# Optimization experiments

Measured on AMD Instinct MI355X. Metric: run time of the kernel, lower is better.

## Reference

```python
import jax, jax.numpy as jnp
import numpy as np

B, N, D = 4, 2048, 512
H, DH = 8, 64
MLP = 2048
EPS = 1e-5


def setup_inputs() -> dict:
    key = jax.random.key(0)
    ks = jax.random.split(key, 8)
    s = lambda fan_in: 1.0 / np.sqrt(fan_in)
    return {
        "x": jax.random.normal(ks[0], (B, N, D), jnp.float32),
        "ln1_g": jnp.ones((D,), jnp.float32),
        "ln1_b": jnp.zeros((D,), jnp.float32),
        "Wqkv": jax.random.normal(ks[1], (D, 3 * H * DH), jnp.float32) * s(D),
        "temperature": jnp.asarray(np.log(DH ** -0.5), jnp.float32),
        "Wo": jax.random.normal(ks[2], (H * DH, D), jnp.float32) * s(H * DH),
        "bo": jnp.zeros((D,), jnp.float32),
        "ln2_g": jnp.ones((D,), jnp.float32),
        "ln2_b": jnp.zeros((D,), jnp.float32),
        "W1": jax.random.normal(ks[3], (D, MLP), jnp.float32) * s(D),
        "b1": jnp.zeros((MLP,), jnp.float32),
        "W2": jax.random.normal(ks[4], (MLP, D), jnp.float32) * s(MLP),
        "b2": jnp.zeros((D,), jnp.float32),
    }


def _layernorm(x, g, b):
    mu = jnp.mean(x, axis=-1, keepdims=True)
    var = jnp.var(x, axis=-1, keepdims=True)
    return (x - mu) * jax.lax.rsqrt(var + EPS) * g + b


def _lsa(x, Wqkv, temperature, Wo, bo):
    b, n, _ = x.shape
    qkv = x @ Wqkv  # [b, n, 3*H*DH]
    q, k, v = jnp.split(qkv, 3, axis=-1)
    rs = lambda t: t.reshape(b, n, H, DH).transpose(0, 2, 1, 3)  # b h n d
    q, k, v = rs(q), rs(k), rs(v)
    dots = jnp.einsum("bhnd,bhmd->bhnm", q, k) * jnp.exp(temperature)
    mask_value = -jnp.finfo(dots.dtype).max
    eye = jnp.eye(n, dtype=bool)
    dots = jnp.where(eye, mask_value, dots)  # mask diagonal (LSA)
    attn = jax.nn.softmax(dots, axis=-1)
    out = jnp.einsum("bhnm,bhmd->bhnd", attn, v)
    out = out.transpose(0, 2, 1, 3).reshape(b, n, H * DH)
    return out @ Wo + bo


def _ffn(x, W1, b1, W2, b2):
    h = jax.nn.gelu(x @ W1 + b1, approximate=False)
    return h @ W2 + b2


def reference(x, ln1_g, ln1_b, Wqkv, temperature, Wo, bo,
              ln2_g, ln2_b, W1, b1, W2, b2):
    y = _lsa(_layernorm(x, ln1_g, ln1_b), Wqkv, temperature, Wo, bo) + x
    z = _ffn(_layernorm(y, ln2_g, ln2_b), W1, b1, W2, b2) + y
    return (z, x)
```

## Files before the change

### kernel.cpp

```cpp
#include <hip/hip_runtime.h>
#include <math.h>

typedef __attribute__((ext_vector_type(4))) float f32x4;
typedef __attribute__((ext_vector_type(8))) short short8;

#define DEV __device__ __forceinline__

DEV short f2bf(float f){
  union { float f; unsigned u; } v; v.f = f;
  unsigned r = v.u + 0x7fffu + ((v.u >> 16) & 1u);
  return (short)(r >> 16);
}
DEV float bf2f(short s){
  union { unsigned u; float f; } v; v.u = ((unsigned)(unsigned short)s) << 16; return v.f;
}
DEV float exp2_hw(float x){ float r; asm("v_exp_f32 %0, %1" : "=v"(r) : "v"(x)); return r; }
DEV float rcp_hw(float x){ float r; asm("v_rcp_f32 %0, %1" : "=v"(r) : "v"(x)); return r; }
DEV unsigned cvtpk(float a, float b){
  unsigned r; asm("v_cvt_pk_bf16_f32 %0, %1, %2" : "=v"(r) : "v"(a), "v"(b)); return r;
}
DEV void gload_lds16(const short* src, short* lds){
  __builtin_amdgcn_global_load_lds(
      (const __attribute__((address_space(1))) void*)src,
      (__attribute__((address_space(3))) void*)lds, 16, 0, 0);
}
DEV float gelu_fast(float v){
  float u = v * (0.79788456f + 0.03567741f * v * v);
  float e = exp2_hw(u * 2.88539008f);
  float th = 1.0f - 2.0f * rcp_hw(e + 1.0f);
  return 0.5f * v * (1.0f + th);
}

__global__ __launch_bounds__(256) void transpose_bf16_kernel(
    const float* __restrict__ W, short* __restrict__ Wt, int K, int N)
{
  __shared__ float tile[32][33];
  int nb = blockIdx.x * 32, kb = blockIdx.y * 32;
  int tx = threadIdx.x & 31, ty = threadIdx.x >> 5;
  #pragma unroll
  for (int i = ty; i < 32; i += 8)
    tile[i][tx] = W[(size_t)(kb + i) * N + nb + tx];
  __syncthreads();
  #pragma unroll
  for (int i = ty; i < 32; i += 8)
    Wt[(size_t)(nb + i) * K + kb + tx] = f2bf(tile[tx][i]);
}

template<int COPYX>
__global__ __launch_bounds__(256) void ln_kernel(
    const float* __restrict__ x, const float* __restrict__ g,
    const float* __restrict__ b, short* __restrict__ out,
    float* __restrict__ xcopy)
{
  int row  = blockIdx.x * 4 + (threadIdx.x >> 6);
  int lane = threadIdx.x & 63;
  const float* xr = x + (size_t)row * 512 + lane * 8;
  f32x4 v0 = *(const f32x4*)(xr);
  f32x4 v1 = *(const f32x4*)(xr + 4);
  float s  = (v0[0]+v0[1]+v0[2]+v0[3]) + (v1[0]+v1[1]+v1[2]+v1[3]);
  float sq = (v0[0]*v0[0]+v0[1]*v0[1]+v0[2]*v0[2]+v0[3]*v0[3])
           + (v1[0]*v1[0]+v1[1]*v1[1]+v1[2]*v1[2]+v1[3]*v1[3]);
  #pragma unroll
  for (int off = 1; off < 64; off <<= 1) {
    s  += __shfl_xor(s, off);
    sq += __shfl_xor(sq, off);
  }
  float mu  = s * (1.0f / 512.0f);
  float var = sq * (1.0f / 512.0f) - mu * mu;
  float rstd = rsqrtf(var + 1e-5f);
  f32x4 g0 = *(const f32x4*)(g + lane * 8);
  f32x4 g1 = *(const f32x4*)(g + lane * 8 + 4);
  f32x4 b0 = *(const f32x4*)(b + lane * 8);
  f32x4 b1 = *(const f32x4*)(b + lane * 8 + 4);
  float o[8];
  #pragma unroll
  for (int j = 0; j < 4; ++j) o[j]     = (v0[j] - mu) * rstd * g0[j] + b0[j];
  #pragma unroll
  for (int j = 0; j < 4; ++j) o[4 + j] = (v1[j] - mu) * rstd * g1[j] + b1[j];
  uint4 pk;
  pk.x = cvtpk(o[0], o[1]); pk.y = cvtpk(o[2], o[3]);
  pk.z = cvtpk(o[4], o[5]); pk.w = cvtpk(o[6], o[7]);
  *(uint4*)(out + (size_t)row * 512 + lane * 8) = pk;
  if (COPYX) {
    float* xc = xcopy + (size_t)row * 512 + lane * 8;
    *(f32x4*)(xc)     = v0;
    *(f32x4*)(xc + 4) = v1;
  }
}

__global__ __launch_bounds__(256) void ln_bf_kernel(
    const short* __restrict__ x, const float* __restrict__ g,
    const float* __restrict__ b, short* __restrict__ out)
{
  int row  = blockIdx.x * 4 + (threadIdx.x >> 6);
  int lane = threadIdx.x & 63;
  short8 raw = *(const short8*)(x + (size_t)row * 512 + lane * 8);
  float v[8];
  #pragma unroll
  for (int j = 0; j < 8; ++j) v[j] = bf2f(raw[j]);
  float s = 0.f, sq = 0.f;
  #pragma unroll
  for (int j = 0; j < 8; ++j) { s += v[j]; sq += v[j] * v[j]; }
  #pragma unroll
  for (int off = 1; off < 64; off <<= 1) {
    s  += __shfl_xor(s, off);
    sq += __shfl_xor(sq, off);
  }
  float mu  = s * (1.0f / 512.0f);
  float var = sq * (1.0f / 512.0f) - mu * mu;
  float rstd = rsqrtf(var + 1e-5f);
  f32x4 g0 = *(const f32x4*)(g + lane * 8);
  f32x4 g1 = *(const f32x4*)(g + lane * 8 + 4);
  f32x4 b0 = *(const f32x4*)(b + lane * 8);
  f32x4 b1 = *(const f32x4*)(b + lane * 8 + 4);
  float o[8];
  #pragma unroll
  for (int j = 0; j < 4; ++j) o[j]     = (v[j] - mu) * rstd * g0[j] + b0[j];
  #pragma unroll
  for (int j = 0; j < 4; ++j) o[4 + j] = (v[4+j] - mu) * rstd * g1[j] + b1[j];
  uint4 pk;
  pk.x = cvtpk(o[0], o[1]); pk.y = cvtpk(o[2], o[3]);
  pk.z = cvtpk(o[4], o[5]); pk.w = cvtpk(o[6], o[7]);
  *(uint4*)(out + (size_t)row * 512 + lane * 8) = pk;
}

template<int EPI, int BM, typename OutT>
__global__ __launch_bounds__(256) void gemm_bt_kernel(
    const short* __restrict__ A, const short* __restrict__ Bt,
    OutT* __restrict__ C, const float* __restrict__ bias,
    const float* __restrict__ resid, const short* __restrict__ residb,
    short* __restrict__ vt, int M, int N, int K)
{
  constexpr int MFR = BM / 32;
  constexpr int NFR = 4;
  constexpr int AI  = BM / 64;
  constexpr int BUF = BM * 32 + 128 * 32;
  __shared__ __align__(16) short smem[3 * BUF];

  int tid = threadIdx.x;
  int lane = tid & 63, wid = tid >> 6;
  int l16 = lane & 15, lq = lane >> 4;

  int gx = gridDim.x;
  int nwg = gx * gridDim.y;
  int orig = blockIdx.y * gx + blockIdx.x;
  int swz = (orig & 7) * (nwg >> 3) + (orig >> 3);
  int bn = swz % gx, bm = swz / gx;

  int wm = wid >> 1, wn = wid & 1;

  const short* gaP[AI];
  const short* gbP[2];
  #pragma unroll
  for (int i = 0; i < AI; ++i) {
    int gg = i * 4 + wid;
    gaP[i] = A + (size_t)(bm * BM + gg * 16 + l16) * K + lq * 8;
  }
  #pragma unroll
  for (int i = 0; i < 2; ++i) {
    int gg = i * 4 + wid;
    gbP[i] = Bt + (size_t)(bn * 128 + gg * 16 + l16) * K + lq * 8;
  }

  auto STAGE = [&](int bufi, int k0) {
    short* base = smem + bufi * BUF;
    #pragma unroll
    for (int i = 0; i < AI; ++i)
      gload_lds16(gaP[i] + k0, base + (i * 4 + wid) * 512);
    #pragma unroll
    for (int i = 0; i < 2; ++i)
      gload_lds16(gbP[i] + k0, base + BM * 32 + (i * 4 + wid) * 512);
  };

  f32x4 acc[MFR][NFR] = {};

  STAGE(0, 0);
  STAGE(1, 32);

  int nt = K >> 5;
  for (int t = 0; t < nt; ++t) {
    if (t + 1 < nt) {
      if constexpr (AI == 2) asm volatile("s_waitcnt vmcnt(4)" ::: "memory");
      else                   asm volatile("s_waitcnt vmcnt(3)" ::: "memory");
    } else {
      asm volatile("s_waitcnt vmcnt(0)" ::: "memory");
    }
    __builtin_amdgcn_s_barrier();
    __builtin_amdgcn_sched_barrier(0);
    if (t + 2 < nt) STAGE((t + 2) % 3, (t + 2) << 5);

    const short* base = smem + (t % 3) * BUF;
    short8 af[MFR], bfr[NFR];
    #pragma unroll
    for (int m = 0; m < MFR; ++m)
      af[m] = *(const short8*)(base + (wm * MFR + m) * 512 + lane * 8);
    #pragma unroll
    for (int n = 0; n < NFR; ++n)
      bfr[n] = *(const short8*)(base + BM * 32 + (wn * NFR + n) * 512 + lane * 8);
    __builtin_amdgcn_s_setprio(1);
    #pragma unroll
    for (int m = 0; m < MFR; ++m)
      #pragma unroll
      for (int n = 0; n < NFR; ++n)
        acc[m][n] = __builtin_amdgcn_mfma_f32_16x16x32_bf16(af[m], bfr[n], acc[m][n], 0, 0, 0);
    __builtin_amdgcn_s_setprio(0);
  }

  if (EPI == 3 && bn >= 8) {
    __syncthreads();
    short* T = smem;
    #pragma unroll
    for (int m = 0; m < MFR; ++m)
      #pragma unroll
      for (int n = 0; n < NFR; ++n) {
        int c = wn * 64 + n * 16 + l16;
        #pragma unroll
        for (int r = 0; r < 4; ++r) {
          int rowl = wm * 64 + m * 16 + lq * 4 + r;
          T[c * 128 + (rowl ^ ((c & 7) << 4))] = f2bf(acc[m][n][r]);
        }
      }
    __syncthreads();
    int b2 = bm >> 4;
    int nnb = (bm & 15) * 128;
    int tn = tid & 15;
    #pragma unroll
    for (int c8 = 0; c8 < 8; ++c8) {
      int c = c8 * 16 + (tid >> 4);
      short8 v = *(const short8*)(T + c * 128 + ((tn * 8) ^ ((c & 7) << 4)));
      if (tn & 1) {
        short8 w;
        #pragma unroll
        for (int j = 0; j < 8; ++j) w[j] = v[j ^ 4];
        v = w;
      }
      int c2 = bn * 128 + c - 1024;
      int bh = b2 * 8 + (c2 >> 6);
      int d  = c2 & 63;
      *(short8*)(vt + ((size_t)(bh * 64 + d)) * 2048 + nnb + tn * 8) = v;
    }
    return;
  }

  float bv[NFR];
  #pragma unroll
  for (int n = 0; n < NFR; ++n)
    bv[n] = (EPI == 0 || EPI == 3) ? 0.0f : bias[bn * 128 + (wn * NFR + n) * 16 + l16];

  #pragma unroll
  for (int m = 0; m < MFR; ++m) {
    #pragma unroll
    for (int r = 0; r < 4; ++r) {
      int row = bm * BM + (wm * MFR + m) * 16 + lq * 4 + r;
      #pragma unroll
      for (int n = 0; n < NFR; ++n) {
        int col = bn * 128 + (wn * NFR + n) * 16 + l16;
        float v = acc[m][n][r];
        if (EPI == 2 || EPI == 4 || EPI == 5) v += bv[n];
        if (EPI == 2) v = gelu_fast(v);
        if (EPI == 4) v += resid[(size_t)row * N + col];
        if (EPI == 5) v += bf2f(residb[(size_t)row * N + col]);
        if constexpr (sizeof(OutT) == 2)
          ((short*)C)[(size_t)row * N + col] = f2bf(v);
        else
          ((float*)C)[(size_t)row * N + col] = v;
      }
    }
  }
}

__global__ __launch_bounds__(256, 2) void attn_kernel(
    const short* __restrict__ qkv, const short* __restrict__ vt,
    const float* __restrict__ temp_ptr,
    short* __restrict__ Op0, short* __restrict__ Op1, float* __restrict__ Lbuf)
{
  __shared__ __align__(16) short smem[16384];

  int tid = threadIdx.x;
  int lane = tid & 63, wid = tid >> 6;
  int l16 = lane & 15, lq = lane >> 4;
  int hi = lq >> 1, lq0 = lq & 1;

  int orig = blockIdx.y * 16 + blockIdx.x;
  int swz = (orig & 7) * 128 + (orig >> 3);
  int qb = swz & 15;
  int rr = swz >> 4;
  int bh = rr & 31, slice = rr >> 5;
  int b = bh >> 3, h = bh & 7;

  const short* qbase = qkv + (size_t)b * 2048 * 1536 + h * 64;
  const short* kbase = qbase + 512;
  const short* vbase = vt + (size_t)bh * 64 * 2048;
  int kslice = slice * 1024;

  float scale = __expf(temp_ptr[0]) * 1.44269504f;
  int q0 = qb * 128 + wid * 32;

  short8 qfrag[2][2];
  #pragma unroll
  for (int qf = 0; qf < 2; ++qf) {
    int qrow = q0 + qf * 16 + l16;
    #pragma unroll
    for (int c = 0; c < 2; ++c) {
      short8 raw = *(const short8*)(qbase + (size_t)qrow * 1536 + c * 32 + lq * 8);
      short8 sc;
      #pragma unroll
      for (int j = 0; j < 8; ++j) sc[j] = f2bf(bf2f(raw[j]) * scale);
      qfrag[qf][c] = sc;
    }
  }

  f32x4 accO[2][4] = {};
  float l[2] = {0.f, 0.f};

  auto STAGE = [&](int bufi, int k0) {
    #pragma unroll
    for (int i = 0; i < 2; ++i) {
      int w16 = i * 256 + tid;
      int sub = w16 >> 7;
      int cc  = (w16 >> 6) & 1;
      int lq2 = (w16 >> 4) & 3;
      int l2  = w16 & 15;
      const short* srcK = kbase + (size_t)(k0 + sub * 16 + l2) * 1536 + cc * 32 + lq2 * 8;
      gload_lds16(srcK, smem + bufi * 4096 + (i * 4 + wid) * 512);
      const short* srcV = vbase + (size_t)(sub * 16 + l2) * 2048 + k0 + cc * 32 + lq2 * 8;
      gload_lds16(srcV, smem + 8192 + bufi * 4096 + (i * 4 + wid) * 512);
    }
  };

  STAGE(0, kslice);
  asm volatile("s_waitcnt vmcnt(0)");
  __syncthreads();

  for (int t = 0; t < 16; ++t) {
    int cur = t & 1;
    int k0 = kslice + t * 64;
    if (t + 1 < 16) STAGE(cur ^ 1, k0 + 64);

    const short* kls = smem + cur * 4096;
    const short* vls = smem + 8192 + cur * 4096;

    f32x4 accS[2][4] = {};
    #pragma unroll
    for (int s = 0; s < 4; ++s) {
      short8 kf0 = *(const short8*)(kls + (s * 2 + 0) * 512 + lane * 8);
      short8 kf1 = *(const short8*)(kls + (s * 2 + 1) * 512 + lane * 8);
      #pragma unroll
      for (int qf = 0; qf < 2; ++qf) {
        accS[qf][s] = __builtin_amdgcn_mfma_f32_16x16x32_bf16(kf0, qfrag[qf][0], accS[qf][s], 0, 0, 0);
        accS[qf][s] = __builtin_amdgcn_mfma_f32_16x16x32_bf16(kf1, qfrag[qf][1], accS[qf][s], 0, 0, 0);
      }
    }

    if ((q0 & ~63) == k0) {
      #pragma unroll
      for (int qf = 0; qf < 2; ++qf) {
        int qg = q0 + qf * 16 + l16;
        #pragma unroll
        for (int s = 0; s < 4; ++s)
          #pragma unroll
          for (int r = 0; r < 4; ++r)
            if (k0 + s * 16 + lq * 4 + r == qg) accS[qf][s][r] = -30000.f;
      }
    }

    short8 pa[2][2];
    #pragma unroll
    for (int qf = 0; qf < 2; ++qf) {
      float sum = 0.f;
      unsigned W[4][2];
      #pragma unroll
      for (int s = 0; s < 4; ++s) {
        float p0 = exp2_hw(accS[qf][s][0]);
        float p1 = exp2_hw(accS[qf][s][1]);
        float p2 = exp2_hw(accS[qf][s][2]);
        float p3 = exp2_hw(accS[qf][s][3]);
        sum += (p0 + p1) + (p2 + p3);
        W[s][0] = cvtpk(p0, p1);
        W[s][1] = cvtpk(p2, p3);
      }
      sum += __shfl_xor(sum, 16);
      sum += __shfl_xor(sum, 32);
      l[qf] += sum;

      unsigned K0[2], S0[2], K2[2], S2[2], R0[2], R2[2];
      #pragma unroll
      for (int w = 0; w < 2; ++w) {
        K0[w] = hi ? W[1][w] : W[0][w];
        S0[w] = hi ? W[0][w] : W[1][w];
        K2[w] = hi ? W[3][w] : W[2][w];
        S2[w] = hi ? W[2][w] : W[3][w];
      }
      #pragma unroll
      for (int w = 0; w < 2; ++w) {
        R0[w] = (unsigned)__shfl_xor((int)S0[w], 32);
        R2[w] = (unsigned)__shfl_xor((int)S2[w], 32);
      }
      bool sw = (hi != lq0);
      unsigned FA[2], FB[2], sA[2], sB[2], GA[2], GB[2];
      #pragma unroll
      for (int w = 0; w < 2; ++w) {
        sA[w] = sw ? K0[w] : R0[w];  FA[w] = sw ? R0[w] : K0[w];
        sB[w] = sw ? K2[w] : R2[w];  FB[w] = sw ? R2[w] : K2[w];
      }
      #pragma unroll
      for (int w = 0; w < 2; ++w) {
        GA[w] = (unsigned)__shfl_xor((int)sA[w], 16);
        GB[w] = (unsigned)__shfl_xor((int)sB[w], 16);
      }
      union { unsigned u[4]; short8 s8; } p0u, p1u;
      p0u.u[0] = FA[0]; p0u.u[1] = FA[1]; p0u.u[2] = GA[0]; p0u.u[3] = GA[1];
      p1u.u[0] = FB[0]; p1u.u[1] = FB[1]; p1u.u[2] = GB[0]; p1u.u[3] = GB[1];
      pa[qf][0] = p0u.s8;
      pa[qf][1] = p1u.s8;
    }

    short8 vfr[4][2];
    #pragma unroll
    for (int d = 0; d < 4; ++d) {
      vfr[d][0] = *(const short8*)(vls + (d * 2 + 0) * 512 + lane * 8);
      vfr[d][1] = *(const short8*)(vls + (d * 2 + 1) * 512 + lane * 8);
    }
    #pragma unroll
    for (int qf = 0; qf < 2; ++qf)
      #pragma unroll
      for (int d = 0; d < 4; ++d) {
        accO[qf][d] = __builtin_amdgcn_mfma_f32_16x16x32_bf16(vfr[d][0], pa[qf][0], accO[qf][d], 0, 0, 0);
        accO[qf][d] = __builtin_amdgcn_mfma_f32_16x16x32_bf16(vfr[d][1], pa[qf][1], accO[qf][d], 0, 0, 0);
      }

    __syncthreads();
  }

  short* op = slice ? Op1 : Op0;
  #pragma unroll
  for (int qf = 0; qf < 2; ++qf) {
    int qg = q0 + qf * 16 + l16;
    if (lq == 0) Lbuf[(size_t)(slice * 32 + bh) * 2048 + qg] = l[qf];
    size_t rowoff = (size_t)(b * 2048 + qg) * 512 + h * 64;
    #pragma unroll
    for (int d = 0; d < 4; ++d) {
      unsigned w0 = cvtpk(accO[qf][d][0], accO[qf][d][1]);
      unsigned w1 = cvtpk(accO[qf][d][2], accO[qf][d][3]);
      uint2 pk; pk.x = w0; pk.y = w1;
      *(uint2*)(op + rowoff + d * 16 + lq * 4) = pk;
    }
  }
}

__global__ __launch_bounds__(256) void attn_combine_kernel(
    const short* __restrict__ Op0, const short* __restrict__ Op1,
    const float* __restrict__ Lbuf, short* __restrict__ out)
{
  int idx = blockIdx.x * 256 + threadIdx.x;
  size_t e = (size_t)idx * 8;
  int row = (int)(e >> 9);
  int col = (int)(e & 511);
  int b = row >> 11, q = row & 2047;
  int bh = b * 8 + (col >> 6);
  float l0 = Lbuf[(size_t)bh * 2048 + q];
  float l1 = Lbuf[(size_t)(32 + bh) * 2048 + q];
  float inv = rcp_hw(l0 + l1);
  short8 a = *(const short8*)(Op0 + e);
  short8 c = *(const short8*)(Op1 + e);
  float o[8];
  #pragma unroll
  for (int j = 0; j < 8; ++j) o[j] = (bf2f(a[j]) + bf2f(c[j])) * inv;
  uint4 pk;
  pk.x = cvtpk(o[0], o[1]); pk.y = cvtpk(o[2], o[3]);
  pk.z = cvtpk(o[4], o[5]); pk.w = cvtpk(o[6], o[7]);
  *(uint4*)(out + e) = pk;
}

extern "C" void kernel_launch(void* const* d_in, const int* in_sizes, int n_in,
                              void* d_out, int out_size, void* d_ws, size_t ws_size,
                              hipStream_t stream)
{
  const float* x    = (const float*)d_in[0];
  const float* ln1g = (const float*)d_in[1];
  const float* ln1b = (const float*)d_in[2];
  const float* Wqkv = (const float*)d_in[3];
  const float* temp = (const float*)d_in[4];
  const float* Wo   = (const float*)d_in[5];
  const float* bo   = (const float*)d_in[6];
  const float* ln2g = (const float*)d_in[7];
  const float* ln2b = (const float*)d_in[8];
  const float* W1   = (const float*)d_in[9];
  const float* b1   = (const float*)d_in[10];
  const float* W2   = (const float*)d_in[11];
  const float* b2   = (const float*)d_in[12];
  float* out = (float*)d_out;

  char* ws = (char*)d_ws;
  short* wqkv_t = (short*)(ws);
  float* lpart  = (float*)(ws);
  short* wo_t   = (short*)(ws + 1572864);
  short* w1_t   = (short*)(ws + 2097152);
  short* w2_t   = (short*)(ws + 4194304);
  short* h      = (short*)(ws + 6291456);
  short* qkv    = (short*)(ws + 14680064);
  short* attn   = (short*)(ws + 39845888);
  short* ybf    = (short*)(ws + 48234496);
  short* vt     = (short*)(ws + 48234496);
  short* t      = (short*)(ws + 14680064);

  const int M = 8192;

  transpose_bf16_kernel<<<dim3(1536 / 32, 512 / 32),  256, 0, stream>>>(Wqkv, wqkv_t, 512, 1536);
  transpose_bf16_kernel<<<dim3(512 / 32, 512 / 32),   256, 0, stream>>>(Wo,   wo_t,   512, 512);
  transpose_bf16_kernel<<<dim3(2048 / 32, 512 / 32),  256, 0, stream>>>(W1,   w1_t,   512, 2048);
  transpose_bf16_kernel<<<dim3(512 / 32, 2048 / 32),  256, 0, stream>>>(W2,   w2_t,   2048, 512);

  ln_kernel<1><<<M / 4, 256, 0, stream>>>(x, ln1g, ln1b, h, out + (size_t)M * 512);

  gemm_bt_kernel<3, 128, short><<<dim3(1536 / 128, M / 128), 256, 0, stream>>>(
      h, wqkv_t, qkv, nullptr, nullptr, nullptr, vt, M, 1536, 512);

  attn_kernel<<<dim3(16, 64), 256, 0, stream>>>(qkv, vt, temp, attn, h, lpart);
  attn_combine_kernel<<<M * 512 / 8 / 256, 256, 0, stream>>>(attn, h, lpart, attn);

  gemm_bt_kernel<4, 64, short><<<dim3(512 / 128, M / 64), 256, 0, stream>>>(
      attn, wo_t, ybf, bo, x, nullptr, nullptr, M, 512, 512);

  ln_bf_kernel<<<M / 4, 256, 0, stream>>>(ybf, ln2g, ln2b, h);

  gemm_bt_kernel<2, 128, short><<<dim3(2048 / 128, M / 128), 256, 0, stream>>>(
      h, w1_t, t, b1, nullptr, nullptr, nullptr, M, 2048, 512);

  gemm_bt_kernel<5, 64, float><<<dim3(512 / 128, M / 64), 256, 0, stream>>>(
      t, w2_t, out, b2, nullptr, ybf, nullptr, M, 512, 2048);
}
```

Before: 210.1 us.

## Add 256x128-tile, 512-thread GEMM kernel for QKV and FFN1 projections

Adds a new GEMM kernel with 256x128 output tiles, 8 waves and a K-step of 64 with triple-buffered LDS staging. It is used for the QKV projection (including the V-transpose epilogue) and for the FFN up-projection with GELU. The old kernel keeps only the bias and residual epilogues. Larger tiles raise arithmetic intensity and cut per-iteration barriers, at the cost of more LDS (about 144KB per block), which limits occupancy to one block per CU, and fewer workgroups.

```diff
diff --git a/kernel.cpp b/kernel.cpp
--- a/kernel.cpp
+++ b/kernel.cpp
@@ -129,7 +129,7 @@
     const short* __restrict__ A, const short* __restrict__ Bt,
     OutT* __restrict__ C, const float* __restrict__ bias,
     const float* __restrict__ resid, const short* __restrict__ residb,
-    short* __restrict__ vt, int M, int N, int K)
+    int M, int N, int K)
 {
   constexpr int MFR = BM / 32;
   constexpr int NFR = 4;
@@ -206,46 +206,10 @@
     __builtin_amdgcn_s_setprio(0);
   }
 
-  if (EPI == 3 && bn >= 8) {
-    __syncthreads();
-    short* T = smem;
-    #pragma unroll
-    for (int m = 0; m < MFR; ++m)
-      #pragma unroll
-      for (int n = 0; n < NFR; ++n) {
-        int c = wn * 64 + n * 16 + l16;
-        #pragma unroll
-        for (int r = 0; r < 4; ++r) {
-          int rowl = wm * 64 + m * 16 + lq * 4 + r;
-          T[c * 128 + (rowl ^ ((c & 7) << 4))] = f2bf(acc[m][n][r]);
-        }
-      }
-    __syncthreads();
-    int b2 = bm >> 4;
-    int nnb = (bm & 15) * 128;
-    int tn = tid & 15;
-    #pragma unroll
-    for (int c8 = 0; c8 < 8; ++c8) {
-      int c = c8 * 16 + (tid >> 4);
-      short8 v = *(const short8*)(T + c * 128 + ((tn * 8) ^ ((c & 7) << 4)));
-      if (tn & 1) {
-        short8 w;
-        #pragma unroll
-        for (int j = 0; j < 8; ++j) w[j] = v[j ^ 4];
-        v = w;
-      }
-      int c2 = bn * 128 + c - 1024;
-      int bh = b2 * 8 + (c2 >> 6);
-      int d  = c2 & 63;
-      *(short8*)(vt + ((size_t)(bh * 64 + d)) * 2048 + nnb + tn * 8) = v;
-    }
-    return;
-  }
-
   float bv[NFR];
   #pragma unroll
   for (int n = 0; n < NFR; ++n)
-    bv[n] = (EPI == 0 || EPI == 3) ? 0.0f : bias[bn * 128 + (wn * NFR + n) * 16 + l16];
+    bv[n] = bias[bn * 128 + (wn * NFR + n) * 16 + l16];
 
   #pragma unroll
   for (int m = 0; m < MFR; ++m) {
@@ -255,15 +219,147 @@
       #pragma unroll
       for (int n = 0; n < NFR; ++n) {
         int col = bn * 128 + (wn * NFR + n) * 16 + l16;
-        float v = acc[m][n][r];
-        if (EPI == 2 || EPI == 4 || EPI == 5) v += bv[n];
-        if (EPI == 2) v = gelu_fast(v);
+        float v = acc[m][n][r] + bv[n];
         if (EPI == 4) v += resid[(size_t)row * N + col];
         if (EPI == 5) v += bf2f(residb[(size_t)row * N + col]);
         if constexpr (sizeof(OutT) == 2)
           ((short*)C)[(size_t)row * N + col] = f2bf(v);
         else
           ((float*)C)[(size_t)row * N + col] = v;
+      }
+    }
+  }
+}
+
+template<int EPI>
+__global__ __launch_bounds__(512) void gemm256_kernel(
+    const short* __restrict__ A, const short* __restrict__ Bt,
+    short* __restrict__ C, const float* __restrict__ bias,
+    short* __restrict__ vt, int M, int N, int K)
+{
+  constexpr int BUF = 24576;
+  __shared__ __align__(16) short smem[3 * BUF];
+
+  int tid = threadIdx.x;
+  int lane = tid & 63, wid = tid >> 6;
+  int l16 = lane & 15, lq = lane >> 4;
+
+  int gx = gridDim.x;
+  int nwg = gx * gridDim.y;
+  int orig = blockIdx.y * gx + blockIdx.x;
+  int swz = (orig & 7) * (nwg >> 3) + (orig >> 3);
+  int bn = swz % gx, bm = swz / gx;
+
+  int wm = wid >> 1, wn = wid & 1;
+
+  const short* gaP[4];
+  const short* gbP[2];
+  #pragma unroll
+  for (int i = 0; i < 4; ++i) {
+    int g = i * 8 + wid;
+    gaP[i] = A + (size_t)(bm * 256 + (g >> 1) * 16 + l16) * K + (g & 1) * 32 + lq * 8;
+  }
+  #pragma unroll
+  for (int i = 0; i < 2; ++i) {
+    int g = i * 8 + wid;
+    gbP[i] = Bt + (size_t)(bn * 128 + (g >> 1) * 16 + l16) * K + (g & 1) * 32 + lq * 8;
+  }
+
+  auto STAGE = [&](int bufi, int k0) {
+    short* base = smem + bufi * BUF;
+    #pragma unroll
+    for (int i = 0; i < 4; ++i)
+      gload_lds16(gaP[i] + k0, base + (i * 8 + wid) * 512);
+    #pragma unroll
+    for (int i = 0; i < 2; ++i)
+      gload_lds16(gbP[i] + k0, base + 16384 + (i * 8 + wid) * 512);
+  };
+
+  f32x4 acc[4][4] = {};
+
+  STAGE(0, 0);
+  STAGE(1, 64);
+
+  int nt = K >> 6;
+  for (int t = 0; t < nt; ++t) {
+    if (t + 1 < nt) asm volatile("s_waitcnt vmcnt(6)" ::: "memory");
+    else            asm volatile("s_waitcnt vmcnt(0)" ::: "memory");
+    __builtin_amdgcn_s_barrier();
+    __builtin_amdgcn_sched_barrier(0);
+    if (t + 2 < nt) STAGE((t + 2) % 3, (t + 2) << 6);
+
+    const short* base = smem + (t % 3) * BUF;
+    #pragma unroll
+    for (int kc = 0; kc < 2; ++kc) {
+      short8 af[4], bfr[4];
+      #pragma unroll
+      for (int m = 0; m < 4; ++m)
+        af[m] = *(const short8*)(base + ((wm * 4 + m) * 2 + kc) * 512 + lane * 8);
+      #pragma unroll
+      for (int n = 0; n < 4; ++n)
+        bfr[n] = *(const short8*)(base + 16384 + ((wn * 4 + n) * 2 + kc) * 512 + lane * 8);
+      __builtin_amdgcn_s_setprio(1);
+      #pragma unroll
+      for (int m = 0; m < 4; ++m)
+        #pragma unroll
+        for (int n = 0; n < 4; ++n)
+          acc[m][n] = __builtin_amdgcn_mfma_f32_16x16x32_bf16(af[m], bfr[n], acc[m][n], 0, 0, 0);
+      __builtin_amdgcn_s_setprio(0);
+    }
+  }
+
+  if (EPI == 3 && bn >= 8) {
+    __syncthreads();
+    short* T = smem;
+    #pragma unroll
+    for (int m = 0; m < 4; ++m)
+      #pragma unroll
+      for (int n = 0; n < 4; ++n) {
+        int c = wn * 64 + n * 16 + l16;
+        #pragma unroll
+        for (int r = 0; r < 4; ++r) {
+          int rowl = wm * 64 + m * 16 + lq * 4 + r;
+          T[c * 256 + (rowl ^ ((c & 7) << 4))] = f2bf(acc[m][n][r]);
+        }
+      }
+    __syncthreads();
+    int b2 = bm >> 3;
+    int nnb = (bm & 7) * 256;
+    int tn = tid & 31, cw = tid >> 5;
+    #pragma unroll
+    for (int c8 = 0; c8 < 8; ++c8) {
+      int c = c8 * 16 + cw;
+      short8 v = *(const short8*)(T + c * 256 + ((tn * 8) ^ ((c & 7) << 4)));
+      if (tn & 1) {
+        short8 w;
+        #pragma unroll
+        for (int j = 0; j < 8; ++j) w[j] = v[j ^ 4];
+        v = w;
+      }
+      int c2 = bn * 128 + c - 1024;
+      int bh = b2 * 8 + (c2 >> 6);
+      int d  = c2 & 63;
+      *(short8*)(vt + ((size_t)(bh * 64 + d)) * 2048 + nnb + tn * 8) = v;
+    }
+    return;
+  }
+
+  float bv[4];
+  #pragma unroll
+  for (int n = 0; n < 4; ++n)
+    bv[n] = (EPI == 2) ? bias[bn * 128 + (wn * 4 + n) * 16 + l16] : 0.0f;
+
+  #pragma unroll
+  for (int m = 0; m < 4; ++m) {
+    #pragma unroll
+    for (int r = 0; r < 4; ++r) {
+      int row = bm * 256 + (wm * 4 + m) * 16 + lq * 4 + r;
+      #pragma unroll
+      for (int n = 0; n < 4; ++n) {
+        int col = bn * 128 + (wn * 4 + n) * 16 + l16;
+        float v = acc[m][n][r];
+        if (EPI == 2) v = gelu_fast(v + bv[n]);
+        C[(size_t)row * N + col] = f2bf(v);
       }
     }
   }
@@ -513,20 +609,20 @@
 
   ln_kernel<1><<<M / 4, 256, 0, stream>>>(x, ln1g, ln1b, h, out + (size_t)M * 512);
 
-  gemm_bt_kernel<3, 128, short><<<dim3(1536 / 128, M / 128), 256, 0, stream>>>(
-      h, wqkv_t, qkv, nullptr, nullptr, nullptr, vt, M, 1536, 512);
+  gemm256_kernel<3><<<dim3(1536 / 128, M / 256), 512, 0, stream>>>(
+      h, wqkv_t, qkv, nullptr, vt, M, 1536, 512);
 
   attn_kernel<<<dim3(16, 64), 256, 0, stream>>>(qkv, vt, temp, attn, h, lpart);
   attn_combine_kernel<<<M * 512 / 8 / 256, 256, 0, stream>>>(attn, h, lpart, attn);
 
   gemm_bt_kernel<4, 64, short><<<dim3(512 / 128, M / 64), 256, 0, stream>>>(
-      attn, wo_t, ybf, bo, x, nullptr, nullptr, M, 512, 512);
+      attn, wo_t, ybf, bo, x, nullptr, M, 512, 512);
 
   ln_bf_kernel<<<M / 4, 256, 0, stream>>>(ybf, ln2g, ln2b, h);
 
-  gemm_bt_kernel<2, 128, short><<<dim3(2048 / 128, M / 128), 256, 0, stream>>>(
-      h, w1_t, t, b1, nullptr, nullptr, nullptr, M, 2048, 512);
+  gemm256_kernel<2><<<dim3(2048 / 128, M / 256), 512, 0, stream>>>(
+      h, w1_t, t, b1, nullptr, M, 2048, 512);
 
   gemm_bt_kernel<5, 64, float><<<dim3(512 / 128, M / 64), 256, 0, stream>>>(
-      t, w2_t, out, b2, nullptr, ybf, nullptr, M, 512, 2048);
-}
+      t, w2_t, out, b2, nullptr, ybf, M, 512, 2048);
+}
```

New measurement: 210.8 us. No clear change (+0.4%).
